# Kernel tuning notes

Measured on AMD Instinct MI355X. Metric: run time of the kernel, lower is better.

Reference implementation:

```python
import jax, jax.numpy as jnp
import numpy as np

EPS = 1e-12
TEMP = 0.05
LAMBDA2 = 0.5


def _normalize(x):
    # F.normalize(x, dim=1), eps=1e-12
    n = jnp.linalg.norm(x, axis=1, keepdims=True)
    return x / jnp.maximum(n, EPS)


def _cdist(x, f):
    # torch.cdist p=2: [B, N] euclidean distances
    x2 = jnp.sum(x * x, axis=1, keepdims=True)          # [B,1]
    f2 = jnp.sum(f * f, axis=1)[None, :]                # [1,N]
    d2 = x2 + f2 - 2.0 * (x @ f.T)
    return jnp.sqrt(jnp.maximum(d2, 0.0))


def _ce(logits, targets):
    # F.cross_entropy with integer targets, mean reduction
    logp = jax.nn.log_softmax(logits, axis=1)
    return -jnp.take_along_axis(logp, targets[:, None], axis=1).mean()


def _branch_loss(x_raw, f, targets):
    x = _normalize(x_raw)
    # note: original applies cross_entropy (which does another log_softmax)
    # on top of softmax(cdist(...)) -- reproduced faithfully
    soft = jax.nn.softmax(_cdist(x, f), axis=1)
    out = (x @ f.T) / TEMP
    return _ce(out, targets) + _ce(soft, targets)


def setup_inputs() -> dict:
    key = jax.random.key(0)
    ks = jax.random.split(key, 7)
    B, N, D = 256, 8192, 2048
    inputs = jax.random.normal(ks[0], (B, D), dtype=jnp.float32)
    inputs_up = jax.random.normal(ks[1], (B, D), dtype=jnp.float32)
    inputs_down = jax.random.normal(ks[2], (B, D), dtype=jnp.float32)
    targets = jax.random.randint(ks[3], (B,), 0, N)
    # memory banks are buffers; initialize as L2-normalized rows (realistic state)
    features = _normalize(jax.random.normal(ks[4], (N, D), dtype=jnp.float32))
    features_up = _normalize(jax.random.normal(ks[5], (N, D), dtype=jnp.float32))
    features_down = _normalize(jax.random.normal(ks[6], (N, D), dtype=jnp.float32))
    return {
        "inputs": inputs,
        "inputs_up": inputs_up,
        "inputs_down": inputs_down,
        "targets": targets,
        "epoch": 10,
        "features": features,
        "features_up": features_up,
        "features_down": features_down,
    }


def reference(inputs, inputs_up, inputs_down, targets, epoch, features, features_up, features_down):
    l_mid = _branch_loss(inputs, features, targets)
    l_up = _branch_loss(inputs_up, features_up, targets)
    l_down = _branch_loss(inputs_down, features_down, targets)
    loss = (1.0 - LAMBDA2) * l_mid + LAMBDA2 * (l_up + l_down)
    return loss
```

## Files before the change

kernel.cpp:

```cpp
#include <hip/hip_runtime.h>

typedef float f4v __attribute__((ext_vector_type(4)));
typedef float f32x4 __attribute__((ext_vector_type(4)));
typedef __bf16 bf16x8 __attribute__((ext_vector_type(8)));
typedef unsigned short ushort8 __attribute__((ext_vector_type(8)));
typedef unsigned short us4v __attribute__((ext_vector_type(4)));

static constexpr int KDIM = 2048;

static constexpr size_t OFF_XN      = 0;
static constexpr size_t OFF_PART    = (size_t)3 * 256 * 2048 * 2;
static constexpr size_t OFF_DOTT    = OFF_PART + (size_t)768 * 256 * 16;
static constexpr size_t OFF_ROWLOSS = OFF_DOTT + 768 * 4;

__device__ __forceinline__ unsigned short f2bf(float x) {
  union { float f; unsigned u; } c; c.f = x;
  unsigned r = c.u + 0x7fffu + ((c.u >> 16) & 1u);
  return (unsigned short)(r >> 16);
}

__device__ __forceinline__ void gload_lds16(const void* g, void* l) {
  __builtin_amdgcn_global_load_lds((const __attribute__((address_space(1))) void*)g,
                                   (__attribute__((address_space(3))) void*)l,
                                   16, 0, 0);
}

__global__ __launch_bounds__(256) void k_normalize(
    const float* __restrict__ x0, const float* __restrict__ x1, const float* __restrict__ x2,
    unsigned short* __restrict__ xn)
{
  int bid = blockIdx.x;
  int branch = bid >> 8;
  int row = bid & 255;
  const float* src = (branch == 0 ? x0 : (branch == 1 ? x1 : x2)) + (size_t)row * KDIM;
  int tid = threadIdx.x;
  f4v a = *(const f4v*)(src + tid * 8);
  f4v b = *(const f4v*)(src + tid * 8 + 4);
  float s = a[0]*a[0] + a[1]*a[1] + a[2]*a[2] + a[3]*a[3]
          + b[0]*b[0] + b[1]*b[1] + b[2]*b[2] + b[3]*b[3];
  #pragma unroll
  for (int m = 1; m < 64; m <<= 1) s += __shfl_xor(s, m);
  __shared__ float ls[4];
  if ((tid & 63) == 0) ls[tid >> 6] = s;
  __syncthreads();
  float total = ls[0] + ls[1] + ls[2] + ls[3];
  float inv = 1.0f / fmaxf(sqrtf(total), 1e-12f);
  ushort8 u;
  #pragma unroll
  for (int e = 0; e < 4; ++e) u[e]     = f2bf(a[e] * inv);
  #pragma unroll
  for (int e = 0; e < 4; ++e) u[4 + e] = f2bf(b[e] * inv);
  *(ushort8*)(xn + (size_t)bid * KDIM + tid * 8) = u;
}

__global__ __launch_bounds__(256, 3) void k_gemm_fused(
    const unsigned short* __restrict__ xn,
    const float* __restrict__ f0, const float* __restrict__ f1, const float* __restrict__ f2,
    const int* __restrict__ targets,
    float* __restrict__ part, float* __restrict__ dotT)
{
  __shared__ char lds[2 * 24576];

  int bid = blockIdx.x;
  int swz = (bid & 7) * 96 + (bid >> 3);
  int branch = swz >> 8;
  int ntile = (swz & 255) >> 1;
  int mtile = swz & 1;

  const unsigned short* A = xn + ((size_t)branch * 256 + (size_t)mtile * 128) * KDIM;
  const float* F = (branch == 0 ? f0 : (branch == 1 ? f1 : f2)) + (size_t)ntile * 64 * KDIM;

  int tid = threadIdx.x;
  int wave = tid >> 6;
  int lane = tid & 63;
  int rcol0 = lane & 15;
  int klane = lane >> 4;
  int wr = wave >> 1;
  int wc = wave & 1;

  const unsigned short* aSrc = A + (size_t)(tid >> 3) * KDIM
                             + (((tid & 7) ^ ((tid >> 3) & 7)) << 3);
  char* aDst = lds + (wave * 64) * 16;

#define STAGE_A(kt, buf) do { \
    _Pragma("unroll") for (int g = 0; g < 4; ++g) \
      gload_lds16(aSrc + (size_t)g * 32 * KDIM + (kt) * 64, \
                  aDst + (buf) * 24576 + g * 4096); \
  } while (0)

  const float* bSrc = F + (size_t)(tid >> 4) * KDIM + (tid & 15) * 4;
  f4v bg0, bg1, bg2, bg3;

#define LOADB_G(kt) do { \
    bg0 = *(const f4v*)(bSrc + (kt) * 64); \
    bg1 = *(const f4v*)(bSrc + 16 * KDIM + (kt) * 64); \
    bg2 = *(const f4v*)(bSrc + 32 * KDIM + (kt) * 64); \
    bg3 = *(const f4v*)(bSrc + 48 * KDIM + (kt) * 64); \
  } while (0)

  int bOff = 16384 + (tid >> 4) * 128
           + (((((tid & 15) >> 1)) ^ ((tid >> 4) & 7)) << 4) + (tid & 1) * 8;

#define WRITE_B(buf) do { \
    us4v v0, v1, v2, v3; \
    _Pragma("unroll") for (int e = 0; e < 4; ++e) { \
      v0[e] = f2bf(bg0[e]); v1[e] = f2bf(bg1[e]); \
      v2[e] = f2bf(bg2[e]); v3[e] = f2bf(bg3[e]); \
    } \
    char* wb = lds + (buf) * 24576 + bOff; \
    *(us4v*)(wb)          = v0; \
    *(us4v*)(wb + 2048)   = v1; \
    *(us4v*)(wb + 4096)   = v2; \
    *(us4v*)(wb + 6144)   = v3; \
  } while (0)

  f32x4 acc[4][2];
  #pragma unroll
  for (int i = 0; i < 4; ++i)
    #pragma unroll
    for (int j = 0; j < 2; ++j)
      #pragma unroll
      for (int q = 0; q < 4; ++q) acc[i][j][q] = 0.0f;

  int sa = rcol0 & 7;
  const char* aRd = lds + (wr * 64 + rcol0) * 128;
  const char* bRd = lds + 16384 + (wc * 32 + rcol0) * 128;

#define COMPUTE(buf) do { \
    const char* ra = aRd + (buf) * 24576; \
    const char* rb = bRd + (buf) * 24576; \
    _Pragma("unroll") for (int ks = 0; ks < 2; ++ks) { \
      int ch = (((ks * 4 + klane) ^ sa) << 4); \
      bf16x8 b0 = *(const bf16x8*)(rb + ch); \
      bf16x8 b1 = *(const bf16x8*)(rb + 2048 + ch); \
      bf16x8 a0 = *(const bf16x8*)(ra + ch); \
      bf16x8 a1 = *(const bf16x8*)(ra + 2048 + ch); \
      bf16x8 a2 = *(const bf16x8*)(ra + 4096 + ch); \
      bf16x8 a3 = *(const bf16x8*)(ra + 6144 + ch); \
      acc[0][0] = __builtin_amdgcn_mfma_f32_16x16x32_bf16(a0, b0, acc[0][0], 0, 0, 0); \
      acc[0][1] = __builtin_amdgcn_mfma_f32_16x16x32_bf16(a0, b1, acc[0][1], 0, 0, 0); \
      acc[1][0] = __builtin_amdgcn_mfma_f32_16x16x32_bf16(a1, b0, acc[1][0], 0, 0, 0); \
      acc[1][1] = __builtin_amdgcn_mfma_f32_16x16x32_bf16(a1, b1, acc[1][1], 0, 0, 0); \
      acc[2][0] = __builtin_amdgcn_mfma_f32_16x16x32_bf16(a2, b0, acc[2][0], 0, 0, 0); \
      acc[2][1] = __builtin_amdgcn_mfma_f32_16x16x32_bf16(a2, b1, acc[2][1], 0, 0, 0); \
      acc[3][0] = __builtin_amdgcn_mfma_f32_16x16x32_bf16(a3, b0, acc[3][0], 0, 0, 0); \
      acc[3][1] = __builtin_amdgcn_mfma_f32_16x16x32_bf16(a3, b1, acc[3][1], 0, 0, 0); \
    } \
  } while (0)

  LOADB_G(0);
  STAGE_A(0, 0);
  WRITE_B(0);
  __syncthreads();

  for (int kt = 0; kt < 32; ++kt) {
    int cur = kt & 1;
    if (kt < 31) {
      LOADB_G(kt + 1);
      STAGE_A(kt + 1, cur ^ 1);
    }
    COMPUTE(cur);
    if (kt < 31) WRITE_B(cur ^ 1);
    __syncthreads();
  }

#undef STAGE_A
#undef LOADB_G
#undef WRITE_B
#undef COMPUTE

  int tbase = branch * 256;
  int mbase = mtile * 128;
  #pragma unroll
  for (int i = 0; i < 4; ++i) {
    #pragma unroll
    for (int q = 0; q < 4; ++q) {
      int row = mbase + wr * 64 + i * 16 + (klane << 2) + q;
      int tgt = targets[row];
      float s1 = 0.f, s2 = 0.f, s3 = 0.f, s4 = 0.f;
      #pragma unroll
      for (int j = 0; j < 2; ++j) {
        float d = acc[i][j][q];
        float e1 = __expf(fmaf(20.0f, d, -20.0f));
        float Dv = sqrtf(fmaxf(2.0f - 2.0f * d, 0.0f));
        float e2 = __expf(Dv - 2.0f);
        s1 += e1; s2 += e2;
        float t2 = e2 * e2;
        s3 += t2; s4 += t2 * e2;
        int col = ntile * 64 + wc * 32 + j * 16 + rcol0;
        if (col == tgt) dotT[tbase + row] = d;
      }
      #pragma unroll
      for (int m = 1; m < 16; m <<= 1) {
        s1 += __shfl_xor(s1, m);
        s2 += __shfl_xor(s2, m);
        s3 += __shfl_xor(s3, m);
        s4 += __shfl_xor(s4, m);
      }
      if (rcol0 == 0) {
        f32x4 p; p[0] = s1; p[1] = s2; p[2] = s3; p[3] = s4;
        *(f32x4*)(part + ((size_t)(tbase + row) * 256 + ntile * 2 + wc) * 4) = p;
      }
    }
  }
}

__global__ __launch_bounds__(256) void k_combine(
    const float* __restrict__ part, const float* __restrict__ dotT, float* __restrict__ rowloss)
{
  int row = blockIdx.x;
  int tid = threadIdx.x;
  f4v p = *(const f4v*)(part + ((size_t)row * 256 + tid) * 4);
  float a0 = p[0], a1 = p[1], a2 = p[2], a3 = p[3];
  #pragma unroll
  for (int m = 1; m < 64; m <<= 1) {
    a0 += __shfl_xor(a0, m); a1 += __shfl_xor(a1, m);
    a2 += __shfl_xor(a2, m); a3 += __shfl_xor(a3, m);
  }
  __shared__ float ls[4][4];
  if ((tid & 63) == 0) {
    int w = tid >> 6;
    ls[0][w] = a0; ls[1][w] = a1; ls[2][w] = a2; ls[3][w] = a3;
  }
  __syncthreads();
  if (tid == 0) {
    float p1 = ls[0][0] + ls[0][1] + ls[0][2] + ls[0][3];
    float Z1 = ls[1][0] + ls[1][1] + ls[1][2] + ls[1][3];
    float Z2 = ls[2][0] + ls[2][1] + ls[2][2] + ls[2][3];
    float Z3 = ls[3][0] + ls[3][1] + ls[3][2] + ls[3][3];
    float dt = dotT[row];
    float CE1 = 20.0f + logf(p1) - 20.0f * dt;
    float Dt = sqrtf(fmaxf(2.0f - 2.0f * dt, 0.0f));
    float St = __expf(Dt - 2.0f) / Z1;
    float sES = 8193.0f + Z2 / (2.0f * Z1 * Z1) + Z3 / (6.0f * Z1 * Z1 * Z1);
    float CE2 = logf(sES) - St;
    rowloss[row] = (CE1 + CE2) * (0.5f / 256.0f);
  }
}

__global__ __launch_bounds__(256) void k_final(const float* __restrict__ rowloss, float* __restrict__ out)
{
  int tid = threadIdx.x;
  float v = rowloss[tid] + rowloss[tid + 256] + rowloss[tid + 512];
  #pragma unroll
  for (int m = 1; m < 64; m <<= 1) v += __shfl_xor(v, m);
  __shared__ float ls[4];
  if ((tid & 63) == 0) ls[tid >> 6] = v;
  __syncthreads();
  if (tid == 0) out[0] = ls[0] + ls[1] + ls[2] + ls[3];
}

extern "C" void kernel_launch(void* const* d_in, const int* in_sizes, int n_in,
                              void* d_out, int out_size, void* d_ws, size_t ws_size,
                              hipStream_t stream) {
  const float* in0 = (const float*)d_in[0];
  const float* in1 = (const float*)d_in[1];
  const float* in2 = (const float*)d_in[2];
  const int* targets = (const int*)d_in[3];
  const float* f0 = (const float*)d_in[5];
  const float* f1 = (const float*)d_in[6];
  const float* f2 = (const float*)d_in[7];

  char* ws = (char*)d_ws;
  unsigned short* xn = (unsigned short*)(ws + OFF_XN);
  float* part    = (float*)(ws + OFF_PART);
  float* dotT    = (float*)(ws + OFF_DOTT);
  float* rowloss = (float*)(ws + OFF_ROWLOSS);
  float* out = (float*)d_out;

  k_normalize<<<768, 256, 0, stream>>>(in0, in1, in2, xn);
  k_gemm_fused<<<768, 256, 0, stream>>>(xn, f0, f1, f2, targets, part, dotT);
  k_combine<<<768, 256, 0, stream>>>(part, dotT, rowloss);
  k_final<<<1, 256, 0, stream>>>(rowloss, out);
}
```

Measured before the change: 70.76 us.

## Prefetch B tiles two stages ahead with manual waitcnt and hardware bf16 convert

Reworks the GEMM main loop into an unrolled two-phase pipeline. Register loads of the fp32 feature tile are issued two K-steps ahead, and the previous registers are written to LDS before compute. Barriers use explicit s_waitcnt vmcnt(4) plus sched_barrier instead of __syncthreads, so outstanding global loads can stay in flight across the barrier. The manual round-to-nearest bf16 conversion is replaced with native __bf16 casts. This costs extra registers for the second prefetch set, and the hand-written waitcnt counts must match the number of in-flight loads to stay correct.

```diff
diff --git a/kernel.cpp b/kernel.cpp
--- a/kernel.cpp
+++ b/kernel.cpp
@@ -3,8 +3,8 @@
 typedef float f4v __attribute__((ext_vector_type(4)));
 typedef float f32x4 __attribute__((ext_vector_type(4)));
 typedef __bf16 bf16x8 __attribute__((ext_vector_type(8)));
+typedef __bf16 bf16x4 __attribute__((ext_vector_type(4)));
 typedef unsigned short ushort8 __attribute__((ext_vector_type(8)));
-typedef unsigned short us4v __attribute__((ext_vector_type(4)));
 
 static constexpr int KDIM = 2048;
 
@@ -23,6 +23,12 @@
   __builtin_amdgcn_global_load_lds((const __attribute__((address_space(1))) void*)g,
                                    (__attribute__((address_space(3))) void*)l,
                                    16, 0, 0);
+}
+
+__device__ __forceinline__ void cvt_store8(char* p, f4v v) {
+  bf16x4 o;
+  o[0] = (__bf16)v[0]; o[1] = (__bf16)v[1]; o[2] = (__bf16)v[2]; o[3] = (__bf16)v[3];
+  *(bf16x4*)p = o;
 }
 
 __global__ __launch_bounds__(256) void k_normalize(
@@ -89,29 +95,23 @@
   } while (0)
 
   const float* bSrc = F + (size_t)(tid >> 4) * KDIM + (tid & 15) * 4;
-  f4v bg0, bg1, bg2, bg3;
-
-#define LOADB_G(kt) do { \
-    bg0 = *(const f4v*)(bSrc + (kt) * 64); \
-    bg1 = *(const f4v*)(bSrc + 16 * KDIM + (kt) * 64); \
-    bg2 = *(const f4v*)(bSrc + 32 * KDIM + (kt) * 64); \
-    bg3 = *(const f4v*)(bSrc + 48 * KDIM + (kt) * 64); \
+
+#define LOADB_G(kt, r0, r1, r2, r3) do { \
+    r0 = *(const f4v*)(bSrc + (kt) * 64); \
+    r1 = *(const f4v*)(bSrc + 16 * KDIM + (kt) * 64); \
+    r2 = *(const f4v*)(bSrc + 32 * KDIM + (kt) * 64); \
+    r3 = *(const f4v*)(bSrc + 48 * KDIM + (kt) * 64); \
   } while (0)
 
   int bOff = 16384 + (tid >> 4) * 128
            + (((((tid & 15) >> 1)) ^ ((tid >> 4) & 7)) << 4) + (tid & 1) * 8;
 
-#define WRITE_B(buf) do { \
-    us4v v0, v1, v2, v3; \
-    _Pragma("unroll") for (int e = 0; e < 4; ++e) { \
-      v0[e] = f2bf(bg0[e]); v1[e] = f2bf(bg1[e]); \
-      v2[e] = f2bf(bg2[e]); v3[e] = f2bf(bg3[e]); \
-    } \
+#define WRITE_B(r0, r1, r2, r3, buf) do { \
     char* wb = lds + (buf) * 24576 + bOff; \
-    *(us4v*)(wb)          = v0; \
-    *(us4v*)(wb + 2048)   = v1; \
-    *(us4v*)(wb + 4096)   = v2; \
-    *(us4v*)(wb + 6144)   = v3; \
+    cvt_store8(wb,         r0); \
+    cvt_store8(wb + 2048,  r1); \
+    cvt_store8(wb + 4096,  r2); \
+    cvt_store8(wb + 6144,  r3); \
   } while (0)
 
   f32x4 acc[4][2];
@@ -148,26 +148,49 @@
     } \
   } while (0)
 
-  LOADB_G(0);
+#define PHASE_END_4() do { \
+    asm volatile("s_waitcnt vmcnt(4) lgkmcnt(0)" ::: "memory"); \
+    __builtin_amdgcn_s_barrier(); \
+    __builtin_amdgcn_sched_barrier(0); \
+  } while (0)
+
+  f4v pA0, pA1, pA2, pA3;
+  f4v pB0, pB1, pB2, pB3;
+
   STAGE_A(0, 0);
-  WRITE_B(0);
-  __syncthreads();
-
-  for (int kt = 0; kt < 32; ++kt) {
-    int cur = kt & 1;
-    if (kt < 31) {
-      LOADB_G(kt + 1);
-      STAGE_A(kt + 1, cur ^ 1);
-    }
-    COMPUTE(cur);
-    if (kt < 31) WRITE_B(cur ^ 1);
-    __syncthreads();
-  }
+  __builtin_amdgcn_sched_barrier(0);
+  LOADB_G(0, pA0, pA1, pA2, pA3);
+  LOADB_G(1, pB0, pB1, pB2, pB3);
+  WRITE_B(pA0, pA1, pA2, pA3, 0);
+  PHASE_END_4();
+
+  for (int t = 0; t < 30; t += 2) {
+    STAGE_A(t + 1, 1);
+    __builtin_amdgcn_sched_barrier(0);
+    LOADB_G(t + 2, pA0, pA1, pA2, pA3);
+    WRITE_B(pB0, pB1, pB2, pB3, 1);
+    COMPUTE(0);
+    PHASE_END_4();
+    STAGE_A(t + 2, 0);
+    __builtin_amdgcn_sched_barrier(0);
+    LOADB_G(t + 3, pB0, pB1, pB2, pB3);
+    WRITE_B(pA0, pA1, pA2, pA3, 0);
+    COMPUTE(1);
+    PHASE_END_4();
+  }
+  STAGE_A(31, 1);
+  WRITE_B(pB0, pB1, pB2, pB3, 1);
+  COMPUTE(0);
+  asm volatile("s_waitcnt vmcnt(0) lgkmcnt(0)" ::: "memory");
+  __builtin_amdgcn_s_barrier();
+  __builtin_amdgcn_sched_barrier(0);
+  COMPUTE(1);
 
 #undef STAGE_A
 #undef LOADB_G
 #undef WRITE_B
 #undef COMPUTE
+#undef PHASE_END_4
 
   int tbase = branch * 256;
   int mbase = mtile * 128;
```

Measured after the change: 65.89 us. -6.9%, faster.

## Stream fp32 feature tiles directly into LDS with smaller M tiles

Applied to the files above, without the earlier changes.

The fused GEMM now stages the fp32 feature tile straight into LDS with global_load_lds and converts it to bf16 when reading it for the MFMAs. This replaces the old path that loaded B into registers, converted it, and wrote it to LDS. The M tile drops from 128 to 64 rows, LDS is single-buffered, and the grid doubles to 1536 blocks with an occupancy hint of 6. The aim is to remove register staging and raise occupancy. In exchange, each feature tile is read twice as often, the fp32 data takes more LDS space, and the load/compute double-buffer overlap is gone.

```diff
diff --git a/kernel.cpp b/kernel.cpp
--- a/kernel.cpp
+++ b/kernel.cpp
@@ -3,8 +3,8 @@
 typedef float f4v __attribute__((ext_vector_type(4)));
 typedef float f32x4 __attribute__((ext_vector_type(4)));
 typedef __bf16 bf16x8 __attribute__((ext_vector_type(8)));
+typedef __bf16 bf16x4 __attribute__((ext_vector_type(4)));
 typedef unsigned short ushort8 __attribute__((ext_vector_type(8)));
-typedef unsigned short us4v __attribute__((ext_vector_type(4)));
 
 static constexpr int KDIM = 2048;
 
@@ -25,6 +25,13 @@
                                    16, 0, 0);
 }
 
+__device__ __forceinline__ bf16x8 cvt8(f4v lo, f4v hi) {
+  bf16x8 r;
+  r[0] = (__bf16)lo[0]; r[1] = (__bf16)lo[1]; r[2] = (__bf16)lo[2]; r[3] = (__bf16)lo[3];
+  r[4] = (__bf16)hi[0]; r[5] = (__bf16)hi[1]; r[6] = (__bf16)hi[2]; r[7] = (__bf16)hi[3];
+  return r;
+}
+
 __global__ __launch_bounds__(256) void k_normalize(
     const float* __restrict__ x0, const float* __restrict__ x1, const float* __restrict__ x2,
     unsigned short* __restrict__ xn)
@@ -53,21 +60,22 @@
   *(ushort8*)(xn + (size_t)bid * KDIM + tid * 8) = u;
 }
 
-__global__ __launch_bounds__(256, 3) void k_gemm_fused(
+__global__ __launch_bounds__(256, 6) void k_gemm_fused(
     const unsigned short* __restrict__ xn,
     const float* __restrict__ f0, const float* __restrict__ f1, const float* __restrict__ f2,
     const int* __restrict__ targets,
     float* __restrict__ part, float* __restrict__ dotT)
 {
-  __shared__ char lds[2 * 24576];
+  __shared__ char lds[24576];
 
   int bid = blockIdx.x;
-  int swz = (bid & 7) * 96 + (bid >> 3);
-  int branch = swz >> 8;
-  int ntile = (swz & 255) >> 1;
-  int mtile = swz & 1;
-
-  const unsigned short* A = xn + ((size_t)branch * 256 + (size_t)mtile * 128) * KDIM;
+  int swz = (bid & 7) * 192 + (bid >> 3);
+  int branch = swz >> 9;
+  int rem = swz & 511;
+  int ntile = rem >> 2;
+  int mtile = rem & 3;
+
+  const unsigned short* A = xn + ((size_t)branch * 256 + (size_t)mtile * 64) * KDIM;
   const float* F = (branch == 0 ? f0 : (branch == 1 ? f1 : f2)) + (size_t)ntile * 64 * KDIM;
 
   int tid = threadIdx.x;
@@ -80,102 +88,71 @@
 
   const unsigned short* aSrc = A + (size_t)(tid >> 3) * KDIM
                              + (((tid & 7) ^ ((tid >> 3) & 7)) << 3);
-  char* aDst = lds + (wave * 64) * 16;
-
-#define STAGE_A(kt, buf) do { \
+  const float* bSrc = F + (size_t)(tid >> 4) * KDIM
+                    + (((tid & 15) ^ ((tid >> 4) & 15)) << 2);
+  char* aDst = lds + wave * 1024;
+  char* bDst = lds + 8192 + wave * 1024;
+
+#define STAGE(kt) do { \
+    gload_lds16(aSrc + (kt) * 64, aDst); \
+    gload_lds16(aSrc + (size_t)32 * KDIM + (kt) * 64, aDst + 4096); \
     _Pragma("unroll") for (int g = 0; g < 4; ++g) \
-      gload_lds16(aSrc + (size_t)g * 32 * KDIM + (kt) * 64, \
-                  aDst + (buf) * 24576 + g * 4096); \
+      gload_lds16(bSrc + (size_t)g * 16 * KDIM + (kt) * 64, bDst + g * 4096); \
   } while (0)
 
-  const float* bSrc = F + (size_t)(tid >> 4) * KDIM + (tid & 15) * 4;
-  f4v bg0, bg1, bg2, bg3;
-
-#define LOADB_G(kt) do { \
-    bg0 = *(const f4v*)(bSrc + (kt) * 64); \
-    bg1 = *(const f4v*)(bSrc + 16 * KDIM + (kt) * 64); \
-    bg2 = *(const f4v*)(bSrc + 32 * KDIM + (kt) * 64); \
-    bg3 = *(const f4v*)(bSrc + 48 * KDIM + (kt) * 64); \
-  } while (0)
-
-  int bOff = 16384 + (tid >> 4) * 128
-           + (((((tid & 15) >> 1)) ^ ((tid >> 4) & 7)) << 4) + (tid & 1) * 8;
-
-#define WRITE_B(buf) do { \
-    us4v v0, v1, v2, v3; \
-    _Pragma("unroll") for (int e = 0; e < 4; ++e) { \
-      v0[e] = f2bf(bg0[e]); v1[e] = f2bf(bg1[e]); \
-      v2[e] = f2bf(bg2[e]); v3[e] = f2bf(bg3[e]); \
-    } \
-    char* wb = lds + (buf) * 24576 + bOff; \
-    *(us4v*)(wb)          = v0; \
-    *(us4v*)(wb + 2048)   = v1; \
-    *(us4v*)(wb + 4096)   = v2; \
-    *(us4v*)(wb + 6144)   = v3; \
-  } while (0)
-
-  f32x4 acc[4][2];
-  #pragma unroll
-  for (int i = 0; i < 4; ++i)
+  f32x4 acc[2][2];
+  #pragma unroll
+  for (int i = 0; i < 2; ++i)
     #pragma unroll
     for (int j = 0; j < 2; ++j)
       #pragma unroll
       for (int q = 0; q < 4; ++q) acc[i][j][q] = 0.0f;
 
   int sa = rcol0 & 7;
-  const char* aRd = lds + (wr * 64 + rcol0) * 128;
-  const char* bRd = lds + 16384 + (wc * 32 + rcol0) * 128;
-
-#define COMPUTE(buf) do { \
-    const char* ra = aRd + (buf) * 24576; \
-    const char* rb = bRd + (buf) * 24576; \
+  const char* aRd = lds + (wr * 32 + rcol0) * 128;
+  const char* bRd = lds + 8192 + (wc * 32 + rcol0) * 256;
+
+#define COMPUTE() do { \
     _Pragma("unroll") for (int ks = 0; ks < 2; ++ks) { \
-      int ch = (((ks * 4 + klane) ^ sa) << 4); \
-      bf16x8 b0 = *(const bf16x8*)(rb + ch); \
-      bf16x8 b1 = *(const bf16x8*)(rb + 2048 + ch); \
-      bf16x8 a0 = *(const bf16x8*)(ra + ch); \
-      bf16x8 a1 = *(const bf16x8*)(ra + 2048 + ch); \
-      bf16x8 a2 = *(const bf16x8*)(ra + 4096 + ch); \
-      bf16x8 a3 = *(const bf16x8*)(ra + 6144 + ch); \
+      int chA = (((ks * 4 + klane) ^ sa) << 4); \
+      int x = ks * 8 + klane * 2; \
+      int chB0 = ((x ^ rcol0) << 4); \
+      int chB1 = (((x + 1) ^ rcol0) << 4); \
+      f4v lo0 = *(const f4v*)(bRd + chB0); \
+      f4v hi0 = *(const f4v*)(bRd + chB1); \
+      f4v lo1 = *(const f4v*)(bRd + 4096 + chB0); \
+      f4v hi1 = *(const f4v*)(bRd + 4096 + chB1); \
+      bf16x8 b0 = cvt8(lo0, hi0); \
+      bf16x8 b1 = cvt8(lo1, hi1); \
+      bf16x8 a0 = *(const bf16x8*)(aRd + chA); \
+      bf16x8 a1 = *(const bf16x8*)(aRd + 2048 + chA); \
       acc[0][0] = __builtin_amdgcn_mfma_f32_16x16x32_bf16(a0, b0, acc[0][0], 0, 0, 0); \
       acc[0][1] = __builtin_amdgcn_mfma_f32_16x16x32_bf16(a0, b1, acc[0][1], 0, 0, 0); \
       acc[1][0] = __builtin_amdgcn_mfma_f32_16x16x32_bf16(a1, b0, acc[1][0], 0, 0, 0); \
       acc[1][1] = __builtin_amdgcn_mfma_f32_16x16x32_bf16(a1, b1, acc[1][1], 0, 0, 0); \
-      acc[2][0] = __builtin_amdgcn_mfma_f32_16x16x32_bf16(a2, b0, acc[2][0], 0, 0, 0); \
-      acc[2][1] = __builtin_amdgcn_mfma_f32_16x16x32_bf16(a2, b1, acc[2][1], 0, 0, 0); \
-      acc[3][0] = __builtin_amdgcn_mfma_f32_16x16x32_bf16(a3, b0, acc[3][0], 0, 0, 0); \
-      acc[3][1] = __builtin_amdgcn_mfma_f32_16x16x32_bf16(a3, b1, acc[3][1], 0, 0, 0); \
     } \
   } while (0)
 
-  LOADB_G(0);
-  STAGE_A(0, 0);
-  WRITE_B(0);
-  __syncthreads();
-
-  for (int kt = 0; kt < 32; ++kt) {
-    int cur = kt & 1;
-    if (kt < 31) {
-      LOADB_G(kt + 1);
-      STAGE_A(kt + 1, cur ^ 1);
-    }
-    COMPUTE(cur);
-    if (kt < 31) WRITE_B(cur ^ 1);
+  STAGE(0);
+  __syncthreads();
+  for (int kt = 0; kt < 31; ++kt) {
+    COMPUTE();
     __syncthreads();
-  }
-
-#undef STAGE_A
-#undef LOADB_G
-#undef WRITE_B
+    STAGE(kt + 1);
+    __syncthreads();
+  }
+  COMPUTE();
+
+#undef STAGE
 #undef COMPUTE
 
   int tbase = branch * 256;
-  int mbase = mtile * 128;
-  #pragma unroll
-  for (int i = 0; i < 4; ++i) {
+  int mbase = mtile * 64;
+  #pragma unroll
+  for (int i = 0; i < 2; ++i) {
     #pragma unroll
     for (int q = 0; q < 4; ++q) {
-      int row = mbase + wr * 64 + i * 16 + (klane << 2) + q;
+      int row = mbase + wr * 32 + i * 16 + (klane << 2) + q;
       int tgt = targets[row];
       float s1 = 0.f, s2 = 0.f, s3 = 0.f, s4 = 0.f;
       #pragma unroll
@@ -269,7 +246,7 @@
   float* out = (float*)d_out;
 
   k_normalize<<<768, 256, 0, stream>>>(in0, in1, in2, xn);
-  k_gemm_fused<<<768, 256, 0, stream>>>(xn, f0, f1, f2, targets, part, dotT);
+  k_gemm_fused<<<1536, 256, 0, stream>>>(xn, f0, f1, f2, targets, part, dotT);
   k_combine<<<768, 256, 0, stream>>>(part, dotT, rowloss);
   k_final<<<1, 256, 0, stream>>>(rowloss, out);
 }
```

After: 79.02 us. 1.12x slower.
